# Kernel optimization log

Measured on AMD Instinct MI355X. Metric: run time of the kernel, lower is better.

Reference implementation:

```python
import jax, jax.numpy as jnp
import numpy as np

B, T, H, V = 2, 1024, 4096, 32000
IGNORE_INDEX = -100
BETA = 0.1


def setup_inputs() -> dict:
    key = jax.random.key(0)
    k = jax.random.split(key, 6)
    scale = 1.0 / np.sqrt(H)  # Linear default init scale
    return {
        "x": jax.random.normal(k[0], (B, T, H), jnp.float32),
        "ref_x": jax.random.normal(k[1], (B, T, H), jnp.float32),
        "y": jax.random.randint(k[2], (B, T), 0, V),
        "preference_labels": jax.random.randint(k[3], (B,), 0, 2).astype(bool),
        "W": jax.random.normal(k[4], (V, H), jnp.float32) * scale,
        "ref_W": jax.random.normal(k[5], (V, H), jnp.float32) * scale,
    }


def _avg_logp(h, W, y):
    # h: (B,T,H), W: (V,H), y: (B,T) -> per-sequence average target log-prob (B,)
    logits = jnp.einsum("bth,vh->btv", h, W)
    logp = jax.nn.log_softmax(logits, axis=-1)
    tok_logp = jnp.take_along_axis(logp, jnp.clip(y, 0, V - 1)[..., None], axis=-1)[..., 0]
    mask = (y != IGNORE_INDEX).astype(tok_logp.dtype)
    # average_log_prob=True: mean over non-ignored tokens
    return jnp.sum(tok_logp * mask, axis=-1) / jnp.maximum(jnp.sum(mask, axis=-1), 1.0)


def reference(x, ref_x, y, preference_labels, W, ref_W):
    policy_logps = _avg_logp(x, W, y)            # (B,)
    ref_logps = _avg_logp(ref_x, ref_W, y)       # (B,), no-grad path in original
    logratios = policy_logps - ref_logps
    multiplier = jnp.where(preference_labels, 1.0, -1.0)
    # KTO loss with kl=None: 1 - sigmoid(beta * logratios * multiplier)
    losses = 1.0 - jax.nn.sigmoid(BETA * logratios * multiplier)
    return jnp.sum(losses) / y.shape[0]
```

## Files before the change

kernel.cpp:

```cpp
#include <hip/hip_runtime.h>
#include <hip/hip_bf16.h>
#include <math.h>

#define TT 1024
#define MM 2048
#define HH 4096
#define VV 32000
#define BETA_ 0.1f
#define NPB (VV/64)

#define BM 256
#define BN 256
#define BK 64
#define NT (HH/BK)

typedef short short8 __attribute__((ext_vector_type(8)));
typedef float f32x4 __attribute__((ext_vector_type(4)));
typedef unsigned u32x2 __attribute__((ext_vector_type(2)));

__device__ inline unsigned f2bf1(float f) {
    union { float f; unsigned u; } v; v.f = f;
    return (v.u + 0x7fffu + ((v.u >> 16) & 1u)) >> 16;
}
__device__ inline uint2 pack4(float4 a) {
    uint2 r;
    r.x = f2bf1(a.x) | (f2bf1(a.y) << 16);
    r.y = f2bf1(a.z) | (f2bf1(a.w) << 16);
    return r;
}
__device__ inline unsigned cvtpk(float lo, float hi) {
    union { __hip_bfloat162 h; unsigned u; } v;
    v.h = __float22bfloat162_rn(make_float2(lo, hi));
    return v.u;
}

__device__ __forceinline__ void gload_lds16(const void* g, void* l) {
    __builtin_amdgcn_global_load_lds(
        (const __attribute__((address_space(1))) void*)(uintptr_t)g,
        (__attribute__((address_space(3))) void*)(unsigned)(uintptr_t)l,
        16, 0, 0);
}

__global__ __launch_bounds__(256) void conv_bf16(
    const float* __restrict__ src, unsigned short* __restrict__ dst, int n8)
{
    int i = blockIdx.x * 256 + threadIdx.x;
    const int stride = gridDim.x * 256;
    for (; i < n8; i += stride) {
        const float4* s = (const float4*)src + 2 * (size_t)i;
        float4 a = s[0], b = s[1];
        uint2 lo = pack4(a), hi = pack4(b);
        *(uint4*)(dst + (size_t)i * 8) = make_uint4(lo.x, lo.y, hi.x, hi.y);
    }
}

template<bool CONV>
__global__ __launch_bounds__(512, 2) void kto_logits_lse_v11(
    const unsigned short* __restrict__ Xb, const unsigned short* __restrict__ Wb,
    float2* __restrict__ part,
    const float* __restrict__ csrc, unsigned short* __restrict__ cdst)
{
    __shared__ __align__(16) unsigned char lds[131072];

    const int tid  = threadIdx.x;
    const int lane = tid & 63;
    const int wave = tid >> 6;
    const int wr   = wave >> 2;
    const int wc   = wave & 3;
    const int lrow = lane & 15;
    const int lgrp = lane >> 4;

    const int fid  = blockIdx.y * gridDim.x + blockIdx.x;
    const int swz  = (fid & 7) * 125 + (fid >> 3);
    const int tile_m = (swz & 7) * BM;
    const int tile_n = (swz >> 3) * BN;

    const int scol = ((lane & 7) * 8) ^ ((lane >> 3) << 3);

    f32x4 acc[8][4];
#pragma unroll
    for (int i = 0; i < 8; ++i)
#pragma unroll
        for (int j = 0; j < 4; ++j) acc[i][j] = f32x4{0.f, 0.f, 0.f, 0.f};

#define STAGE_HALF(S)                                                         \
    do { int s_ = (S);                                                        \
        if (s_ < 4 * NT) {                                                    \
            int ts_ = s_ >> 2, kind_ = s_ & 3, buf_ = ts_ & 1;                \
            int isA_ = kind_ >> 1, half_ = kind_ & 1;                         \
            const unsigned short* base_ = isA_                                \
                ? Xb + (size_t)tile_m * HH : Wb + (size_t)tile_n * HH;        \
            unsigned char* lb_ = lds + (isA_ ? 0 : 65536) + buf_ * 32768;     \
            _Pragma("unroll")                                                 \
            for (int c_ = 0; c_ < 2; ++c_) {                                  \
                int rt_ = half_ * 128 + wave * 16 + c_ * 8;                   \
                gload_lds16(base_ + (size_t)(rt_ + (lane >> 3)) * HH          \
                                  + ts_ * 64 + scol,                          \
                            lb_ + rt_ * 128);                                 \
            }                                                                 \
        } } while (0)

#define LOAD_A(DST, MH)                                                       \
    _Pragma("unroll") for (int m_ = 0; m_ < 4; ++m_)                          \
    _Pragma("unroll") for (int kk_ = 0; kk_ < 2; ++kk_) {                     \
        int rr_ = wr * 128 + (MH) * 64 + m_ * 16 + lrow;                      \
        DST[m_][kk_] = *(const short8*)(ldsAp + rr_ * 128 +                   \
            ((kk_ * 64 + lgrp * 16) ^ ((rr_ & 7) << 4))); }

#define LOAD_B(DST, NH)                                                       \
    _Pragma("unroll") for (int n_ = 0; n_ < 2; ++n_)                          \
    _Pragma("unroll") for (int kk_ = 0; kk_ < 2; ++kk_) {                     \
        int rb_ = wc * 64 + (NH) * 32 + n_ * 16 + lrow;                       \
        DST[n_][kk_] = *(const short8*)(ldsBp + rb_ * 128 +                   \
            ((kk_ * 64 + lgrp * 16) ^ ((rb_ & 7) << 4))); }

#define MFMA16(AF, BF, MB, NB)                                                \
    _Pragma("unroll") for (int m_ = 0; m_ < 4; ++m_)                          \
    _Pragma("unroll") for (int n_ = 0; n_ < 2; ++n_)                          \
    _Pragma("unroll") for (int kk_ = 0; kk_ < 2; ++kk_)                       \
        acc[(MB) + m_][(NB) + n_] = __builtin_amdgcn_mfma_f32_16x16x32_bf16(  \
            AF[m_][kk_], BF[n_][kk_], acc[(MB) + m_][(NB) + n_], 0, 0, 0);

#define SBAR()                                                                \
    __builtin_amdgcn_sched_barrier(0);                                        \
    __builtin_amdgcn_s_barrier();                                             \
    __builtin_amdgcn_sched_barrier(0);

    f32x4 cv, cvn;

#pragma unroll
    for (int s = 0; s < 6; ++s) STAGE_HALF(s);
    if (CONV) {
        cv = __builtin_nontemporal_load(
            (const f32x4*)(csrc + (size_t)fid * NT * 2048 + tid * 4));
        asm volatile("s_waitcnt vmcnt(5)" ::: "memory");
    } else {
        asm volatile("s_waitcnt vmcnt(4)" ::: "memory");
    }
    SBAR();

    for (int t = 0; t < NT; ++t) {
        const int p = t & 1;
        const unsigned char* ldsAp = lds + p * 32768;
        const unsigned char* ldsBp = lds + 65536 + p * 32768;
        short8 afa[4][2], afb[4][2], bfa[2][2], bfb[2][2];

        STAGE_HALF(4 * t + 6);
        STAGE_HALF(4 * t + 7);
        if (CONV && t + 1 < NT)
            cvn = __builtin_nontemporal_load(
                (const f32x4*)(csrc + ((size_t)fid * NT + t + 1) * 2048 + tid * 4));
        LOAD_A(afa, 0);
        LOAD_B(bfa, 0);
        LOAD_B(bfb, 1);
        __builtin_amdgcn_s_setprio(1);
        MFMA16(afa, bfa, 0, 0);
        MFMA16(afa, bfb, 0, 2);
        __builtin_amdgcn_s_setprio(0);
        SBAR();
        STAGE_HALF(4 * t + 8);
        STAGE_HALF(4 * t + 9);
        if (CONV) {
            u32x2 q;
            q[0] = cvtpk(cv[0], cv[1]);
            q[1] = cvtpk(cv[2], cv[3]);
            __builtin_nontemporal_store(q,
                (u32x2*)(cdst + ((size_t)fid * NT + t) * 2048 + tid * 4));
        }
        LOAD_A(afb, 1);
        __builtin_amdgcn_s_setprio(1);
        MFMA16(afb, bfa, 4, 0);
        MFMA16(afb, bfb, 4, 2);
        __builtin_amdgcn_s_setprio(0);
        if (CONV && t + 1 < NT) cv = cvn;
        if (t < NT - 2) {
            if (CONV) { asm volatile("s_waitcnt vmcnt(6)" ::: "memory"); }
            else      { asm volatile("s_waitcnt vmcnt(4)" ::: "memory"); }
        } else        { asm volatile("s_waitcnt vmcnt(0)" ::: "memory"); }
        SBAR();
    }

    const int nb = (tile_n >> 6) + wc;
#pragma unroll
    for (int mi = 0; mi < 8; ++mi) {
#pragma unroll
        for (int r = 0; r < 4; ++r) {
            float v0 = acc[mi][0][r], v1 = acc[mi][1][r], v2 = acc[mi][2][r], v3 = acc[mi][3][r];
            float mx = fmaxf(fmaxf(v0, v1), fmaxf(v2, v3));
#pragma unroll
            for (int d = 1; d < 16; d <<= 1) mx = fmaxf(mx, __shfl_xor(mx, d, 64));
            float s = __expf(v0 - mx) + __expf(v1 - mx) + __expf(v2 - mx) + __expf(v3 - mx);
#pragma unroll
            for (int d = 1; d < 16; d <<= 1) s += __shfl_xor(s, d, 64);
            if (lrow == 0) {
                int rowg = tile_m + wr * 128 + mi * 16 + lgrp * 4 + r;
                part[(size_t)rowg * NPB + nb] = make_float2(mx, s);
            }
        }
    }
}

__global__ __launch_bounds__(256) void kto_logits_lse(
    const float* __restrict__ X, const float* __restrict__ Wt,
    float2* __restrict__ part)
{
    __shared__ __align__(16) unsigned char ldsf[(128 + 128) * BK * 2];
    unsigned char* ldsA = ldsf;
    unsigned char* ldsB = ldsf + 128 * BK * 2;

    const int tid    = threadIdx.x;
    const int tile_m = blockIdx.x * 128;
    const int tile_n = blockIdx.y * 128;
    const int srow   = tid >> 1;
    const int shalf  = tid & 1;
    const int lane   = tid & 63;
    const int wave   = tid >> 6;
    const int wm     = (wave >> 1) * 64;
    const int wn     = (wave & 1) * 64;
    const int lrow   = lane & 15;
    const int lgrp   = lane >> 4;

    f32x4 acc[4][4];
#pragma unroll
    for (int i = 0; i < 4; ++i)
#pragma unroll
        for (int j = 0; j < 4; ++j) acc[i][j] = f32x4{0.f, 0.f, 0.f, 0.f};

    const float4* gA = (const float4*)(X  + (size_t)(tile_m + srow) * HH) + shalf * 8;
    const float4* gB = (const float4*)(Wt + (size_t)(tile_n + srow) * HH) + shalf * 8;
    const int swzf = (srow & 7) << 4;

    for (int k0 = 0; k0 < HH; k0 += BK) {
        float4 a[8], b[8];
#pragma unroll
        for (int j = 0; j < 8; ++j) a[j] = gA[j];
#pragma unroll
        for (int j = 0; j < 8; ++j) b[j] = gB[j];
        gA += BK / 4; gB += BK / 4;

        __syncthreads();
#pragma unroll
        for (int j = 0; j < 4; ++j) {
            uint2 lo = pack4(a[2*j]), hi = pack4(a[2*j+1]);
            uint4 qa = make_uint4(lo.x, lo.y, hi.x, hi.y);
            lo = pack4(b[2*j]); hi = pack4(b[2*j+1]);
            uint4 qb = make_uint4(lo.x, lo.y, hi.x, hi.y);
            int kb = shalf * 64 + 16 * j;
            *(uint4*)(ldsA + srow * 128 + (kb ^ swzf)) = qa;
            *(uint4*)(ldsB + srow * 128 + (kb ^ swzf)) = qb;
        }
        __syncthreads();

#pragma unroll
        for (int kk = 0; kk < 2; ++kk) {
            short8 af[4], bf[4];
#pragma unroll
            for (int mi = 0; mi < 4; ++mi) {
                int r = wm + mi * 16 + lrow;
                af[mi] = *(const short8*)(ldsA + r * 128 + ((kk * 64 + lgrp * 16) ^ ((r & 7) << 4)));
            }
#pragma unroll
            for (int ni = 0; ni < 4; ++ni) {
                int r = wn + ni * 16 + lrow;
                bf[ni] = *(const short8*)(ldsB + r * 128 + ((kk * 64 + lgrp * 16) ^ ((r & 7) << 4)));
            }
#pragma unroll
            for (int mi = 0; mi < 4; ++mi)
#pragma unroll
                for (int ni = 0; ni < 4; ++ni)
                    acc[mi][ni] = __builtin_amdgcn_mfma_f32_16x16x32_bf16(af[mi], bf[ni], acc[mi][ni], 0, 0, 0);
        }
    }

    const int nbf = blockIdx.y * 2 + (wave & 1);
#pragma unroll
    for (int mi = 0; mi < 4; ++mi) {
#pragma unroll
        for (int r = 0; r < 4; ++r) {
            float v0 = acc[mi][0][r], v1 = acc[mi][1][r], v2 = acc[mi][2][r], v3 = acc[mi][3][r];
            float mx = fmaxf(fmaxf(v0, v1), fmaxf(v2, v3));
#pragma unroll
            for (int d = 1; d < 16; d <<= 1) mx = fmaxf(mx, __shfl_xor(mx, d, 64));
            float s = __expf(v0 - mx) + __expf(v1 - mx) + __expf(v2 - mx) + __expf(v3 - mx);
#pragma unroll
            for (int d = 1; d < 16; d <<= 1) s += __shfl_xor(s, d, 64);
            if (lrow == 0) {
                int rowg = tile_m + wm + mi * 16 + lgrp * 4 + r;
                part[(size_t)rowg * NPB + nbf] = make_float2(mx, s);
            }
        }
    }
}

__global__ __launch_bounds__(256) void kto_target(
    const float* __restrict__ X, const float* __restrict__ RX,
    const float* __restrict__ W, const float* __restrict__ RW,
    const int* __restrict__ Y,
    float* __restrict__ tgtP, float* __restrict__ tgtR)
{
    __shared__ float red[2][4];
    const int t = blockIdx.x;
    int yt = Y[t]; yt = yt < 0 ? 0 : (yt > VV - 1 ? VV - 1 : yt);
    const float4* x4  = (const float4*)(X  + (size_t)t  * HH);
    const float4* rx4 = (const float4*)(RX + (size_t)t  * HH);
    const float4* w4  = (const float4*)(W  + (size_t)yt * HH);
    const float4* rw4 = (const float4*)(RW + (size_t)yt * HH);
    float sp = 0.f, sr = 0.f;
    for (int i = threadIdx.x; i < HH / 4; i += 256) {
        float4 a = x4[i],  w = w4[i];
        sp += a.x * w.x + a.y * w.y + a.z * w.z + a.w * w.w;
        float4 bq = rx4[i], rw = rw4[i];
        sr += bq.x * rw.x + bq.y * rw.y + bq.z * rw.z + bq.w * rw.w;
    }
#pragma unroll
    for (int d = 1; d < 64; d <<= 1) { sp += __shfl_xor(sp, d, 64); sr += __shfl_xor(sr, d, 64); }
    int wv = threadIdx.x >> 6, ln = threadIdx.x & 63;
    if (ln == 0) { red[0][wv] = sp; red[1][wv] = sr; }
    __syncthreads();
    if (threadIdx.x == 0) {
        tgtP[t] = red[0][0] + red[0][1] + red[0][2] + red[0][3];
        tgtR[t] = red[1][0] + red[1][1] + red[1][2] + red[1][3];
    }
}

__device__ inline float2 mrg(float2 a, float2 b) {
    if (b.x == -INFINITY) return a;
    if (a.x == -INFINITY) return b;
    if (a.x >= b.x) { a.y += b.y * __expf(b.x - a.x); return a; }
    b.y += a.y * __expf(a.x - b.x); return b;
}

__global__ __launch_bounds__(256) void kto_lse_combine(
    const float2* __restrict__ partP, const float2* __restrict__ partR,
    const float* __restrict__ tgtP, const float* __restrict__ tgtR,
    float* __restrict__ tokP, float* __restrict__ tokR)
{
    __shared__ float2 redP[4], redR[4];
    const int t = blockIdx.x;
    float2 ap = make_float2(-INFINITY, 0.f), ar = ap;
    for (int i = threadIdx.x; i < NPB; i += 256) {
        ap = mrg(ap, partP[(size_t)t * NPB + i]);
        ar = mrg(ar, partR[(size_t)t * NPB + i]);
    }
#pragma unroll
    for (int d = 1; d < 64; d <<= 1) {
        float2 o;
        o.x = __shfl_xor(ap.x, d, 64); o.y = __shfl_xor(ap.y, d, 64); ap = mrg(ap, o);
        o.x = __shfl_xor(ar.x, d, 64); o.y = __shfl_xor(ar.y, d, 64); ar = mrg(ar, o);
    }
    int wv = threadIdx.x >> 6, ln = threadIdx.x & 63;
    if (ln == 0) { redP[wv] = ap; redR[wv] = ar; }
    __syncthreads();
    if (threadIdx.x == 0) {
        float2 p = mrg(mrg(redP[0], redP[1]), mrg(redP[2], redP[3]));
        float2 r = mrg(mrg(redR[0], redR[1]), mrg(redR[2], redR[3]));
        tokP[t] = tgtP[t] - (p.x + logf(p.y));
        tokR[t] = tgtR[t] - (r.x + logf(r.y));
    }
}

__global__ __launch_bounds__(1024) void kto_final(
    const float* __restrict__ tokP, const float* __restrict__ tokR,
    const int* __restrict__ Y, const unsigned char* __restrict__ pref,
    float* __restrict__ out)
{
    __shared__ float red[6][16];
    const int t = threadIdx.x;
    float m0 = (Y[t]      != -100) ? 1.f : 0.f;
    float m1 = (Y[TT + t] != -100) ? 1.f : 0.f;
    float v[6];
    v[0] = m0 * tokP[t];       v[1] = m0 * tokR[t];       v[2] = m0;
    v[3] = m1 * tokP[TT + t];  v[4] = m1 * tokR[TT + t];  v[5] = m1;
#pragma unroll
    for (int d = 1; d < 64; d <<= 1)
#pragma unroll
        for (int j = 0; j < 6; ++j) v[j] += __shfl_xor(v[j], d, 64);
    int wv = threadIdx.x >> 6, ln = threadIdx.x & 63;
    if (ln == 0)
#pragma unroll
        for (int j = 0; j < 6; ++j) red[j][wv] = v[j];
    __syncthreads();
    if (t == 0) {
        float s[6];
#pragma unroll
        for (int j = 0; j < 6; ++j) { s[j] = 0.f; for (int w = 0; w < 16; ++w) s[j] += red[j][w]; }
        bool byteStorage = ((pref[1] | pref[2] | pref[3]) != 0) || (pref[4] > 1) ||
                           ((pref[5] | pref[6] | pref[7]) != 0);
        int l0, l1;
        if (byteStorage) { l0 = pref[0]; l1 = pref[1]; }
        else { l0 = ((const int*)pref)[0]; l1 = ((const int*)pref)[1]; }
        float pl0 = s[0] / fmaxf(s[2], 1.f);
        float rl0 = s[1] / fmaxf(s[2], 1.f);
        float pl1 = s[3] / fmaxf(s[5], 1.f);
        float rl1 = s[4] / fmaxf(s[5], 1.f);
        float lr0 = pl0 - rl0, lr1 = pl1 - rl1;
        float mu0 = l0 ? 1.f : -1.f;
        float mu1 = l1 ? 1.f : -1.f;
        float loss0 = 1.f - 1.f / (1.f + expf(-BETA_ * lr0 * mu0));
        float loss1 = 1.f - 1.f / (1.f + expf(-BETA_ * lr1 * mu1));
        out[0] = 0.5f * (loss0 + loss1);
    }
}

extern "C" void kernel_launch(void* const* d_in, const int* in_sizes, int n_in,
                              void* d_out, int out_size, void* d_ws, size_t ws_size,
                              hipStream_t stream) {
    const float* X  = (const float*)d_in[0];
    const float* RX = (const float*)d_in[1];
    const int*   Y  = (const int*)d_in[2];
    const unsigned char* PL = (const unsigned char*)d_in[3];
    const float* W  = (const float*)d_in[4];
    const float* RW = (const float*)d_in[5];
    float* out = (float*)d_out;

    char* p = (char*)d_ws;
    float2* partP = (float2*)p;                 p += (size_t)MM * NPB * sizeof(float2);
    float2* partR = (float2*)p;                 p += (size_t)MM * NPB * sizeof(float2);
    float*  tgtP  = (float*)p;                  p += MM * sizeof(float);
    float*  tgtR  = (float*)p;                  p += MM * sizeof(float);
    float*  tokP  = (float*)p;                  p += MM * sizeof(float);
    float*  tokR  = (float*)p;                  p += MM * sizeof(float);
    unsigned short* Xbf  = (unsigned short*)p;  p += (size_t)MM * HH * 2;
    unsigned short* RXbf = (unsigned short*)p;  p += (size_t)MM * HH * 2;
    unsigned short* Wbf  = (unsigned short*)p;  p += (size_t)VV * HH * 2;
    const size_t need1 = (size_t)(p - (char*)d_ws);
    unsigned short* RWbf = (unsigned short*)p;  p += (size_t)VV * HH * 2;
    const size_t need2 = (size_t)(p - (char*)d_ws);

    dim3 ggrid(MM / BM, VV / BN);

    if (ws_size >= need2) {
        conv_bf16<<<512,  256, 0, stream>>>(X,  Xbf,  (int)((size_t)MM * HH / 8));
        conv_bf16<<<512,  256, 0, stream>>>(RX, RXbf, (int)((size_t)MM * HH / 8));
        conv_bf16<<<2048, 256, 0, stream>>>(W,  Wbf,  (int)((size_t)VV * HH / 8));
        kto_logits_lse_v11<true ><<<ggrid, 512, 0, stream>>>(Xbf,  Wbf,  partP, RW, RWbf);
        kto_logits_lse_v11<false><<<ggrid, 512, 0, stream>>>(RXbf, RWbf, partR, nullptr, nullptr);
    } else if (ws_size >= need1) {
        conv_bf16<<<512,  256, 0, stream>>>(X,  Xbf,  (int)((size_t)MM * HH / 8));
        conv_bf16<<<512,  256, 0, stream>>>(RX, RXbf, (int)((size_t)MM * HH / 8));
        conv_bf16<<<2048, 256, 0, stream>>>(W,  Wbf,  (int)((size_t)VV * HH / 8));
        kto_logits_lse_v11<false><<<ggrid, 512, 0, stream>>>(Xbf, Wbf, partP, nullptr, nullptr);
        conv_bf16<<<2048, 256, 0, stream>>>(RW, Wbf,  (int)((size_t)VV * HH / 8));
        kto_logits_lse_v11<false><<<ggrid, 512, 0, stream>>>(RXbf, Wbf, partR, nullptr, nullptr);
    } else {
        dim3 fgrid(MM / 128, VV / 128);
        kto_logits_lse<<<fgrid, 256, 0, stream>>>(X,  W,  partP);
        kto_logits_lse<<<fgrid, 256, 0, stream>>>(RX, RW, partR);
    }
    kto_target<<<MM, 256, 0, stream>>>(X, RX, W, RW, Y, tgtP, tgtR);
    kto_lse_combine<<<MM, 256, 0, stream>>>(partP, partR, tgtP, tgtR, tokP, tokR);
    kto_final<<<1, 1024, 0, stream>>>(tokP, tokR, Y, PL, out);
}
```

Baseline: 1.165 ms.

## Load W fragments directly to registers in new GEMM kernel, stage only X in LDS

Adds a v12 logits/LSE GEMM kernel that stages only the activation tile through LDS and loads the weight fragments straight from global memory into registers, double-buffered across k-tiles. This halves LDS usage and removes the LDS round trip and one barrier per k-tile for B. It is used for the reference-model GEMM, and for both GEMMs in the smaller workspace path. In exchange, each wave now issues uncoalesced-ish direct global loads for W, uses more registers, and may see longer load latency exposed per tile.

```diff
diff --git a/kernel.cpp b/kernel.cpp
--- a/kernel.cpp
+++ b/kernel.cpp
@@ -53,6 +53,41 @@
         *(uint4*)(dst + (size_t)i * 8) = make_uint4(lo.x, lo.y, hi.x, hi.y);
     }
 }
+
+#define SBAR()                                                                \
+    __builtin_amdgcn_sched_barrier(0);                                        \
+    __builtin_amdgcn_s_barrier();                                             \
+    __builtin_amdgcn_sched_barrier(0);
+
+#define MFMA16(AF, BF, MB, NB)                                                \
+    _Pragma("unroll") for (int m_ = 0; m_ < 4; ++m_)                          \
+    _Pragma("unroll") for (int n_ = 0; n_ < 2; ++n_)                          \
+    _Pragma("unroll") for (int kk_ = 0; kk_ < 2; ++kk_)                       \
+        acc[(MB) + m_][(NB) + n_] = __builtin_amdgcn_mfma_f32_16x16x32_bf16(  \
+            AF[m_][kk_], BF[n_][kk_], acc[(MB) + m_][(NB) + n_], 0, 0, 0);
+
+#define GEMM_EPILOGUE_256                                                     \
+    const int nb = (tile_n >> 6) + wc;                                        \
+    _Pragma("unroll")                                                         \
+    for (int mi = 0; mi < 8; ++mi) {                                          \
+        _Pragma("unroll")                                                     \
+        for (int r = 0; r < 4; ++r) {                                         \
+            float v0 = acc[mi][0][r], v1 = acc[mi][1][r];                     \
+            float v2 = acc[mi][2][r], v3 = acc[mi][3][r];                     \
+            float mx = fmaxf(fmaxf(v0, v1), fmaxf(v2, v3));                   \
+            _Pragma("unroll")                                                 \
+            for (int d = 1; d < 16; d <<= 1)                                  \
+                mx = fmaxf(mx, __shfl_xor(mx, d, 64));                        \
+            float s = __expf(v0 - mx) + __expf(v1 - mx) +                     \
+                      __expf(v2 - mx) + __expf(v3 - mx);                      \
+            _Pragma("unroll")                                                 \
+            for (int d = 1; d < 16; d <<= 1) s += __shfl_xor(s, d, 64);       \
+            if (lrow == 0) {                                                  \
+                int rowg = tile_m + wr * 128 + mi * 16 + lgrp * 4 + r;        \
+                part[(size_t)rowg * NPB + nb] = make_float2(mx, s);           \
+            }                                                                 \
+        }                                                                     \
+    }
 
 template<bool CONV>
 __global__ __launch_bounds__(512, 2) void kto_logits_lse_v11(
@@ -100,31 +135,19 @@
             }                                                                 \
         } } while (0)
 
-#define LOAD_A(DST, MH)                                                       \
+#define LOAD_A11(DST, MH)                                                     \
     _Pragma("unroll") for (int m_ = 0; m_ < 4; ++m_)                          \
     _Pragma("unroll") for (int kk_ = 0; kk_ < 2; ++kk_) {                     \
         int rr_ = wr * 128 + (MH) * 64 + m_ * 16 + lrow;                      \
         DST[m_][kk_] = *(const short8*)(ldsAp + rr_ * 128 +                   \
             ((kk_ * 64 + lgrp * 16) ^ ((rr_ & 7) << 4))); }
 
-#define LOAD_B(DST, NH)                                                       \
+#define LOAD_B11(DST, NH)                                                     \
     _Pragma("unroll") for (int n_ = 0; n_ < 2; ++n_)                          \
     _Pragma("unroll") for (int kk_ = 0; kk_ < 2; ++kk_) {                     \
         int rb_ = wc * 64 + (NH) * 32 + n_ * 16 + lrow;                       \
         DST[n_][kk_] = *(const short8*)(ldsBp + rb_ * 128 +                   \
             ((kk_ * 64 + lgrp * 16) ^ ((rb_ & 7) << 4))); }
-
-#define MFMA16(AF, BF, MB, NB)                                                \
-    _Pragma("unroll") for (int m_ = 0; m_ < 4; ++m_)                          \
-    _Pragma("unroll") for (int n_ = 0; n_ < 2; ++n_)                          \
-    _Pragma("unroll") for (int kk_ = 0; kk_ < 2; ++kk_)                       \
-        acc[(MB) + m_][(NB) + n_] = __builtin_amdgcn_mfma_f32_16x16x32_bf16(  \
-            AF[m_][kk_], BF[n_][kk_], acc[(MB) + m_][(NB) + n_], 0, 0, 0);
-
-#define SBAR()                                                                \
-    __builtin_amdgcn_sched_barrier(0);                                        \
-    __builtin_amdgcn_s_barrier();                                             \
-    __builtin_amdgcn_sched_barrier(0);
 
     f32x4 cv, cvn;
 
@@ -150,9 +173,9 @@
         if (CONV && t + 1 < NT)
             cvn = __builtin_nontemporal_load(
                 (const f32x4*)(csrc + ((size_t)fid * NT + t + 1) * 2048 + tid * 4));
-        LOAD_A(afa, 0);
-        LOAD_B(bfa, 0);
-        LOAD_B(bfb, 1);
+        LOAD_A11(afa, 0);
+        LOAD_B11(bfa, 0);
+        LOAD_B11(bfb, 1);
         __builtin_amdgcn_s_setprio(1);
         MFMA16(afa, bfa, 0, 0);
         MFMA16(afa, bfb, 0, 2);
@@ -167,7 +190,7 @@
             __builtin_nontemporal_store(q,
                 (u32x2*)(cdst + ((size_t)fid * NT + t) * 2048 + tid * 4));
         }
-        LOAD_A(afb, 1);
+        LOAD_A11(afb, 1);
         __builtin_amdgcn_s_setprio(1);
         MFMA16(afb, bfa, 4, 0);
         MFMA16(afb, bfb, 4, 2);
@@ -180,24 +203,106 @@
         SBAR();
     }
 
-    const int nb = (tile_n >> 6) + wc;
-#pragma unroll
-    for (int mi = 0; mi < 8; ++mi) {
-#pragma unroll
-        for (int r = 0; r < 4; ++r) {
-            float v0 = acc[mi][0][r], v1 = acc[mi][1][r], v2 = acc[mi][2][r], v3 = acc[mi][3][r];
-            float mx = fmaxf(fmaxf(v0, v1), fmaxf(v2, v3));
-#pragma unroll
-            for (int d = 1; d < 16; d <<= 1) mx = fmaxf(mx, __shfl_xor(mx, d, 64));
-            float s = __expf(v0 - mx) + __expf(v1 - mx) + __expf(v2 - mx) + __expf(v3 - mx);
-#pragma unroll
-            for (int d = 1; d < 16; d <<= 1) s += __shfl_xor(s, d, 64);
-            if (lrow == 0) {
-                int rowg = tile_m + wr * 128 + mi * 16 + lgrp * 4 + r;
-                part[(size_t)rowg * NPB + nb] = make_float2(mx, s);
-            }
-        }
-    }
+    GEMM_EPILOGUE_256
+}
+
+__global__ __launch_bounds__(512, 2) void kto_logits_lse_v12(
+    const unsigned short* __restrict__ Xb, const unsigned short* __restrict__ Wb,
+    float2* __restrict__ part)
+{
+    __shared__ __align__(16) unsigned char lds[65536];
+
+    const int tid  = threadIdx.x;
+    const int lane = tid & 63;
+    const int wave = tid >> 6;
+    const int wr   = wave >> 2;
+    const int wc   = wave & 3;
+    const int lrow = lane & 15;
+    const int lgrp = lane >> 4;
+
+    const int fid  = blockIdx.y * gridDim.x + blockIdx.x;
+    const int swz  = (fid & 7) * 125 + (fid >> 3);
+    const int tile_m = (swz & 7) * BM;
+    const int tile_n = (swz >> 3) * BN;
+
+    const int scol = ((lane & 7) * 8) ^ ((lane >> 3) << 3);
+
+    f32x4 acc[8][4];
+#pragma unroll
+    for (int i = 0; i < 8; ++i)
+#pragma unroll
+        for (int j = 0; j < 4; ++j) acc[i][j] = f32x4{0.f, 0.f, 0.f, 0.f};
+
+#define STAGE_A12(T)                                                          \
+    do { int ta_ = (T);                                                       \
+        if (ta_ < NT) {                                                       \
+            unsigned char* la_ = lds + (ta_ & 1) * 32768;                     \
+            _Pragma("unroll")                                                 \
+            for (int h_ = 0; h_ < 2; ++h_)                                    \
+            _Pragma("unroll")                                                 \
+            for (int c_ = 0; c_ < 2; ++c_) {                                  \
+                int rt_ = h_ * 128 + wave * 16 + c_ * 8;                      \
+                gload_lds16(Xb + (size_t)(tile_m + rt_ + (lane >> 3)) * HH    \
+                               + ta_ * 64 + scol,                             \
+                            la_ + rt_ * 128);                                 \
+            }                                                                 \
+        } } while (0)
+
+#define BLOAD12(B0, B1, T)                                                    \
+    do { int tb_ = (T);                                                       \
+        if (tb_ < NT) {                                                       \
+            _Pragma("unroll")                                                 \
+            for (int n_ = 0; n_ < 2; ++n_)                                    \
+            _Pragma("unroll")                                                 \
+            for (int kk_ = 0; kk_ < 2; ++kk_) {                               \
+                B0[n_][kk_] = *(const short8*)(Wb +                           \
+                    (size_t)(tile_n + wc * 64 + n_ * 16 + lrow) * HH          \
+                    + tb_ * 64 + kk_ * 32 + lgrp * 8);                        \
+                B1[n_][kk_] = *(const short8*)(Wb +                           \
+                    (size_t)(tile_n + wc * 64 + 32 + n_ * 16 + lrow) * HH     \
+                    + tb_ * 64 + kk_ * 32 + lgrp * 8);                        \
+            }                                                                 \
+        } } while (0)
+
+#define LOAD_A12(DST, MH)                                                     \
+    _Pragma("unroll") for (int m_ = 0; m_ < 4; ++m_)                          \
+    _Pragma("unroll") for (int kk_ = 0; kk_ < 2; ++kk_) {                     \
+        int rr_ = wr * 128 + (MH) * 64 + m_ * 16 + lrow;                      \
+        DST[m_][kk_] = *(const short8*)(ldsAp + rr_ * 128 +                   \
+            ((kk_ * 64 + lgrp * 16) ^ ((rr_ & 7) << 4))); }
+
+#define TILE12(T, BU0, BU1, BF0, BF1)                                         \
+    do {                                                                      \
+        const unsigned char* ldsAp = lds + ((T) & 1) * 32768;                 \
+        short8 afa[4][2], afb[4][2];                                          \
+        STAGE_A12((T) + 1);                                                   \
+        BLOAD12(BF0, BF1, (T) + 1);                                           \
+        LOAD_A12(afa, 0);                                                     \
+        LOAD_A12(afb, 1);                                                     \
+        __builtin_amdgcn_s_setprio(1);                                        \
+        MFMA16(afa, BU0, 0, 0);                                               \
+        MFMA16(afa, BU1, 0, 2);                                               \
+        MFMA16(afb, BU0, 4, 0);                                               \
+        MFMA16(afb, BU1, 4, 2);                                               \
+        __builtin_amdgcn_s_setprio(0);                                        \
+        if ((T) < NT - 1) { asm volatile("s_waitcnt vmcnt(8)" ::: "memory"); }\
+        else              { asm volatile("s_waitcnt vmcnt(0)" ::: "memory"); }\
+        SBAR();                                                               \
+    } while (0)
+
+    short8 bA0[2][2], bA1[2][2], bB0[2][2], bB1[2][2];
+
+    STAGE_A12(0);
+    BLOAD12(bA0, bA1, 0);
+    asm volatile("s_waitcnt vmcnt(8)" ::: "memory");
+    SBAR();
+
+    for (int t = 0; t < NT; t += 2) {
+        TILE12(t,     bA0, bA1, bB0, bB1);
+        TILE12(t + 1, bB0, bB1, bA0, bA1);
+    }
+
+    GEMM_EPILOGUE_256
 }
 
 __global__ __launch_bounds__(256) void kto_logits_lse(
@@ -433,15 +538,15 @@
         conv_bf16<<<512,  256, 0, stream>>>(X,  Xbf,  (int)((size_t)MM * HH / 8));
         conv_bf16<<<512,  256, 0, stream>>>(RX, RXbf, (int)((size_t)MM * HH / 8));
         conv_bf16<<<2048, 256, 0, stream>>>(W,  Wbf,  (int)((size_t)VV * HH / 8));
-        kto_logits_lse_v11<true ><<<ggrid, 512, 0, stream>>>(Xbf,  Wbf,  partP, RW, RWbf);
-        kto_logits_lse_v11<false><<<ggrid, 512, 0, stream>>>(RXbf, RWbf, partR, nullptr, nullptr);
+        kto_logits_lse_v11<true><<<ggrid, 512, 0, stream>>>(Xbf, Wbf, partP, RW, RWbf);
+        kto_logits_lse_v12<<<ggrid, 512, 0, stream>>>(RXbf, RWbf, partR);
     } else if (ws_size >= need1) {
         conv_bf16<<<512,  256, 0, stream>>>(X,  Xbf,  (int)((size_t)MM * HH / 8));
         conv_bf16<<<512,  256, 0, stream>>>(RX, RXbf, (int)((size_t)MM * HH / 8));
         conv_bf16<<<2048, 256, 0, stream>>>(W,  Wbf,  (int)((size_t)VV * HH / 8));
-        kto_logits_lse_v11<false><<<ggrid, 512, 0, stream>>>(Xbf, Wbf, partP, nullptr, nullptr);
+        kto_logits_lse_v12<<<ggrid, 512, 0, stream>>>(Xbf, Wbf, partP);
         conv_bf16<<<2048, 256, 0, stream>>>(RW, Wbf,  (int)((size_t)VV * HH / 8));
-        kto_logits_lse_v11<false><<<ggrid, 512, 0, stream>>>(RXbf, Wbf, partR, nullptr, nullptr);
+        kto_logits_lse_v12<<<ggrid, 512, 0, stream>>>(RXbf, Wbf, partR);
     } else {
         dim3 fgrid(MM / 128, VV / 128);
         kto_logits_lse<<<fgrid, 256, 0, stream>>>(X,  W,  partP);
```

Result: slower. 2.786 ms (+139.3%).
